# Performance work log

Hardware: AMD Instinct MI355X
Metric: run time of the kernel (lower is better)

The kernel has to match this reference:

```python
import jax, jax.numpy as jnp
import numpy as np

N = 50000
E = 800000
IN_C = 512
HID_C = 128
OUT_C = 16


def setup_inputs() -> dict:
    key = jax.random.key(0)
    k1, k2, k3, k4, k5 = jax.random.split(key, 5)
    x = jax.random.normal(k1, (N, IN_C), dtype=jnp.float32)
    edge_index = jax.random.randint(k2, (2, E), 0, N, dtype=jnp.int64)
    # GCNConv.lin: Linear(in, hid, bias=False); conv bias zero-init but give random for grad coverage
    W1 = jax.random.normal(k3, (HID_C, IN_C), dtype=jnp.float32) / np.sqrt(IN_C)
    b1 = jnp.zeros((HID_C,), dtype=jnp.float32)
    # GCNNet.fc: Linear(hid, out)
    W2 = jax.random.normal(k4, (OUT_C, HID_C), dtype=jnp.float32) / np.sqrt(HID_C)
    b2 = jax.random.normal(k5, (OUT_C,), dtype=jnp.float32) * 0.01
    return {"x": x, "edge_index": edge_index, "W1": W1, "b1": b1, "W2": W2, "b2": b2}


def reference(x, edge_index, W1, b1, W2, b2):
    # Dropout(p=0.5) is identity in eval mode.
    row, col = edge_index[0], edge_index[1]
    h = x @ W1.T                                    # [N, HID_C]
    deg = jax.ops.segment_sum(jnp.ones((E,), dtype=h.dtype), col, num_segments=N)
    # NOTE: source uses deg.pow(0.5) (sqrt, not inv-sqrt) — faithful to the code.
    d = jnp.sqrt(deg)
    norm = d[row] * d[col]                          # [E]
    msg = norm[:, None] * h[row]                    # gather + scale, [E, HID_C]
    agg = jax.ops.segment_sum(msg, col, num_segments=N)  # scatter-add, [N, HID_C]
    conv_out = agg + b1                             # [N, HID_C]
    return conv_out @ W2.T + b2                     # [N, OUT_C]
```

## Files before the change

kernel.cpp:

```cpp
#include <hip/hip_runtime.h>
#include <hip/hip_bf16.h>
#include <hip/hip_fp16.h>

#define IN_C 512
#define HID_C 128
#define OUT_C 16
#define STILE 8192
#define SSH  13
#define KCH_H 16

typedef float    f32x4 __attribute__((ext_vector_type(4)));
typedef float    f32x2 __attribute__((ext_vector_type(2)));
typedef int      i32x4 __attribute__((ext_vector_type(4)));
typedef _Float16 h16x2 __attribute__((ext_vector_type(2)));

__device__ inline void pk_atomic_add_f16(h16x2* addr, h16x2 val) {
#if __has_builtin(__builtin_amdgcn_global_atomic_fadd_v2f16)
    __builtin_amdgcn_global_atomic_fadd_v2f16(addr, val);
#else
    unsigned int* ap = (unsigned int*)addr;
    unsigned int old = *ap, assumed;
    do {
        assumed = old;
        h16x2 cur = __builtin_bit_cast(h16x2, assumed);
        h16x2 nv = cur + val;
        old = atomicCAS(ap, assumed, __builtin_bit_cast(unsigned int, nv));
    } while (old != assumed);
#endif
}

__global__ __launch_bounds__(256) void prep_hist_kernel(
        const float* __restrict__ W1, const float* __restrict__ b1,
        const float* __restrict__ W2, const float* __restrict__ b2,
        float* __restrict__ Wc, float* __restrict__ cconst,
        const int* __restrict__ ei, int* __restrict__ phist, int E) {
    __shared__ int h[STILE];
    if (blockIdx.x < 32) {
        int idx = blockIdx.x * 256 + threadIdx.x;
        int o = idx >> 9;
        int k = idx & 511;
        float s = 0.f;
#pragma unroll 8
        for (int hh = 0; hh < HID_C; ++hh)
            s = fmaf(W2[o * HID_C + hh], W1[hh * IN_C + k], s);
        Wc[o * IN_C + k] = s;
        return;
    }
    if (blockIdx.x == 32) {
        if (threadIdx.x < OUT_C) {
            int o = threadIdx.x;
            float s = b2[o];
            for (int hh = 0; hh < HID_C; ++hh)
                s = fmaf(b1[hh], W2[o * HID_C + hh], s);
            cconst[o] = s;
        }
        return;
    }
    const int hb = blockIdx.x - 33;
    const int st = hb / KCH_H;
    const int k = hb - st * KCH_H;
    for (int i = threadIdx.x; i < STILE; i += 256) h[i] = 0;
    __syncthreads();

    const int chunk = (((E + KCH_H - 1) / KCH_H) + 3) & ~3;
    const int beg = k * chunk;
    const int end = min(E, beg + chunk);
    const int* cols = ei + E;

    const int nv = (end > beg) ? ((end - beg) >> 2) : 0;
    const i32x4* cv = (const i32x4*)(cols + beg);
    for (int i = threadIdx.x; i < nv; i += 256) {
        i32x4 c = cv[i];
#pragma unroll
        for (int j = 0; j < 4; ++j) {
            int cj = c[j];
            if ((cj >> SSH) == st) atomicAdd(&h[cj & (STILE - 1)], 1);
        }
    }
    for (int e = beg + (nv << 2) + threadIdx.x; e < end; e += 256) {
        int cj = cols[e];
        if ((cj >> SSH) == st) atomicAdd(&h[cj & (STILE - 1)], 1);
    }
    __syncthreads();
    int* outp = phist + (size_t)hb * STILE;
    for (int i = threadIdx.x; i < STILE; i += 256) outp[i] = h[i];
}

__global__ void dsq_zero_kernel(const int* __restrict__ phist, float* __restrict__ dsq,
                                unsigned int* __restrict__ agg32, int N, int aggWords) {
    int i = blockIdx.x * 256 + threadIdx.x;
    if (i < N) {
        int st = i >> SSH, ii = i & (STILE - 1);
        const int* p = phist + (size_t)st * KCH_H * STILE + ii;
        int s = 0;
#pragma unroll
        for (int k = 0; k < KCH_H; ++k) s += p[k * STILE];
        dsq[i] = sqrtf((float)s);
    }
    if (i < aggWords) agg32[i] = 0u;
}

__global__ __launch_bounds__(256) void h2_kernel(const float* __restrict__ x,
                                                 const float* __restrict__ WcG,
                                                 const float* __restrict__ dsq,
                                                 _Float16* __restrict__ h2h, int N) {
    __shared__ float wl[16 * IN_C];
    for (int i = threadIdx.x; i < (16 * IN_C) / 4; i += 256)
        ((f32x4*)wl)[i] = ((const f32x4*)WcG)[i];
    __syncthreads();

    const int lane = threadIdx.x & 63;
    const int wid = (blockIdx.x * 256 + threadIdx.x) >> 6;
    const int nw  = (gridDim.x * 256) >> 6;

    for (int r0 = wid * 4; r0 < N; r0 += nw * 4) {
        const int rmax = min(4, N - r0);
        f32x4 a0[4], a1[4];
#pragma unroll
        for (int rr = 0; rr < 4; ++rr) {
            int r = r0 + (rr < rmax ? rr : 0);
            a0[rr] = *(const f32x4*)(x + (size_t)r * IN_C + 4 * lane);
            a1[rr] = *(const f32x4*)(x + (size_t)r * IN_C + 256 + 4 * lane);
        }
        float p[4][16];
#pragma unroll
        for (int oo = 0; oo < 16; ++oo) {
            f32x4 w0 = *(const f32x4*)(wl + oo * IN_C + 4 * lane);
            f32x4 w1 = *(const f32x4*)(wl + oo * IN_C + 256 + 4 * lane);
#pragma unroll
            for (int rr = 0; rr < 4; ++rr) {
                float s = a0[rr].x * w0.x;
                s = fmaf(a0[rr].y, w0.y, s);
                s = fmaf(a0[rr].z, w0.z, s);
                s = fmaf(a0[rr].w, w0.w, s);
                s = fmaf(a1[rr].x, w1.x, s);
                s = fmaf(a1[rr].y, w1.y, s);
                s = fmaf(a1[rr].z, w1.z, s);
                s = fmaf(a1[rr].w, w1.w, s);
                p[rr][oo] = s;
            }
        }
        float v[4];
#pragma unroll
        for (int rr = 0; rr < 4; ++rr) {
#define RSTEP(MASK, HALF)                                              \
            {                                                          \
                const bool hi = (lane & MASK) != 0;                    \
                _Pragma("unroll")                                      \
                for (int ii = 0; ii < HALF; ++ii) {                    \
                    float send = hi ? p[rr][ii] : p[rr][ii + HALF];    \
                    float recv = __shfl_xor(send, MASK, 64);           \
                    float keep = hi ? p[rr][ii + HALF] : p[rr][ii];    \
                    p[rr][ii] = keep + recv;                           \
                }                                                      \
            }
            RSTEP(1, 8)
            RSTEP(2, 4)
            RSTEP(4, 2)
            RSTEP(8, 1)
#undef RSTEP
            v[rr] = p[rr][0];
        }
        const bool h16 = (lane & 16) != 0;
        float sA = h16 ? v[0] : v[1];
        float mA = (h16 ? v[1] : v[0]) + __shfl_xor(sA, 16, 64);
        float sB = h16 ? v[2] : v[3];
        float mB = (h16 ? v[3] : v[2]) + __shfl_xor(sB, 16, 64);
        const bool h32 = (lane & 32) != 0;
        float sC = h32 ? mA : mB;
        float f  = (h32 ? mB : mA) + __shfl_xor(sC, 32, 64);
        const int qq = lane >> 4, jj = lane & 15;
        const int oo = ((jj & 1) << 3) | ((jj & 2) << 1) | ((jj & 4) >> 1) | ((jj & 8) >> 3);
        if (qq < rmax) {
            int r = r0 + qq;
            h2h[(size_t)r * OUT_C + oo] = (_Float16)(f * dsq[r]);
        }
    }
}

__global__ __launch_bounds__(256) void edge_kernel(const int* __restrict__ ei,
                                                   const _Float16* __restrict__ h2h,
                                                   h16x2* __restrict__ agg, int E) {
    int t = blockIdx.x * 256 + threadIdx.x;
    int e = t >> 3;
    if (e >= E) return;
    int op = t & 7;
    int r = ei[e];
    int c = ei[E + e];
    h16x2 h = *(const h16x2*)(h2h + (size_t)r * OUT_C + (op << 1));
    pk_atomic_add_f16(&agg[(size_t)c * 8 + op], h);
}

__global__ void final_kernel(const h16x2* __restrict__ agg, const float* __restrict__ dsq,
                             const float* __restrict__ cconst, float* __restrict__ out,
                             int words) {
    int i = blockIdx.x * 256 + threadIdx.x;
    if (i >= words) return;
    int n = i >> 3;
    int o = (i & 7) << 1;
    h16x2 a = agg[i];
    float d = dsq[n];
    f32x2 r;
    r.x = fmaf(d, (float)a.x, cconst[o]);
    r.y = fmaf(d, (float)a.y, cconst[o + 1]);
    *(f32x2*)(out + ((size_t)i << 1)) = r;
}

extern "C" void kernel_launch(void* const* d_in, const int* in_sizes, int n_in,
                              void* d_out, int out_size, void* d_ws, size_t ws_size,
                              hipStream_t stream) {
    const float* x  = (const float*)d_in[0];
    const int*   ei = (const int*)d_in[1];
    const float* W1 = (const float*)d_in[2];
    const float* b1 = (const float*)d_in[3];
    const float* W2 = (const float*)d_in[4];
    const float* b2 = (const float*)d_in[5];
    float* out = (float*)d_out;

    const int N = in_sizes[0] / IN_C;
    const int E = in_sizes[1] / 2;
    const int ST = (N + STILE - 1) / STILE;
    const int aggWords = (N * OUT_C) / 2;

    float* ws     = (float*)d_ws;
    float* Wc     = ws;
    float* cconst = ws + 16 * IN_C;
    float* dsq    = cconst + 16;
    _Float16* h2h = (_Float16*)(dsq + N);
    int*   phist  = (int*)((unsigned int*)(dsq + N) + 8 * (size_t)N);
    unsigned int* agg32 = (unsigned int*)(phist + (size_t)ST * KCH_H * STILE);
    h16x2* agg = (h16x2*)agg32;

    hipLaunchKernelGGL(prep_hist_kernel, dim3(33 + ST * KCH_H), dim3(256), 0, stream,
                       W1, b1, W2, b2, Wc, cconst, ei, phist, E);
    hipLaunchKernelGGL(dsq_zero_kernel, dim3((aggWords + 255) / 256), dim3(256), 0, stream,
                       phist, dsq, agg32, N, aggWords);
    hipLaunchKernelGGL(h2_kernel, dim3(768), dim3(256), 0, stream, x, Wc, dsq, h2h, N);
    hipLaunchKernelGGL(edge_kernel, dim3((E * 8 + 255) / 256), dim3(256), 0, stream,
                       ei, h2h, agg, E);
    hipLaunchKernelGGL(final_kernel, dim3((aggWords + 255) / 256), dim3(256), 0, stream,
                       agg, dsq, cconst, out, aggWords);
}
```

Before: 101.9 us.

## Fold degree reduction into h2 kernel and agg zeroing into prep launch

Removes the separate dsq_zero kernel. Zeroing of the aggregation buffer moves into extra blocks of the prep/histogram launch. The per-node degree sum and sqrt are now computed inside h2_kernel with a wave shuffle reduction over the partial histograms. The histogram split doubles to 32 chunks and the h2 grid grows, which trades one kernel launch and a dependency for more partial-histogram traffic and extra work inside the GEMV kernel.

```diff
diff --git a/kernel.cpp b/kernel.cpp
--- a/kernel.cpp
+++ b/kernel.cpp
@@ -7,7 +7,7 @@
 #define OUT_C 16
 #define STILE 8192
 #define SSH  13
-#define KCH_H 16
+#define KCH_H 32
 
 typedef float    f32x4 __attribute__((ext_vector_type(4)));
 typedef float    f32x2 __attribute__((ext_vector_type(2)));
@@ -33,7 +33,8 @@
         const float* __restrict__ W1, const float* __restrict__ b1,
         const float* __restrict__ W2, const float* __restrict__ b2,
         float* __restrict__ Wc, float* __restrict__ cconst,
-        const int* __restrict__ ei, int* __restrict__ phist, int E) {
+        const int* __restrict__ ei, int* __restrict__ phist,
+        unsigned int* __restrict__ agg32, int E, int nhist, int aggWords) {
     __shared__ int h[STILE];
     if (blockIdx.x < 32) {
         int idx = blockIdx.x * 256 + threadIdx.x;
@@ -56,6 +57,11 @@
         }
         return;
     }
+    if (blockIdx.x >= 33 + nhist) {
+        int i = (blockIdx.x - 33 - nhist) * 256 + threadIdx.x;
+        if (i < aggWords) agg32[i] = 0u;
+        return;
+    }
     const int hb = blockIdx.x - 33;
     const int st = hb / KCH_H;
     const int k = hb - st * KCH_H;
@@ -86,23 +92,10 @@
     for (int i = threadIdx.x; i < STILE; i += 256) outp[i] = h[i];
 }
 
-__global__ void dsq_zero_kernel(const int* __restrict__ phist, float* __restrict__ dsq,
-                                unsigned int* __restrict__ agg32, int N, int aggWords) {
-    int i = blockIdx.x * 256 + threadIdx.x;
-    if (i < N) {
-        int st = i >> SSH, ii = i & (STILE - 1);
-        const int* p = phist + (size_t)st * KCH_H * STILE + ii;
-        int s = 0;
-#pragma unroll
-        for (int k = 0; k < KCH_H; ++k) s += p[k * STILE];
-        dsq[i] = sqrtf((float)s);
-    }
-    if (i < aggWords) agg32[i] = 0u;
-}
-
 __global__ __launch_bounds__(256) void h2_kernel(const float* __restrict__ x,
                                                  const float* __restrict__ WcG,
-                                                 const float* __restrict__ dsq,
+                                                 const int* __restrict__ phist,
+                                                 float* __restrict__ dsq,
                                                  _Float16* __restrict__ h2h, int N) {
     __shared__ float wl[16 * IN_C];
     for (int i = threadIdx.x; i < (16 * IN_C) / 4; i += 256)
@@ -115,6 +108,20 @@
 
     for (int r0 = wid * 4; r0 < N; r0 += nw * 4) {
         const int rmax = min(4, N - r0);
+
+        const int rr_d = lane >> 4;
+        const int rd = min(r0 + rr_d, N - 1);
+        const int std = rd >> SSH, id = rd & (STILE - 1);
+        const int kd = lane & 15;
+        const int* pb = phist + ((size_t)std * KCH_H) * STILE + id;
+        int deg = pb[(size_t)kd * STILE] + pb[(size_t)(kd + 16) * STILE];
+        deg += __shfl_xor(deg, 1, 64);
+        deg += __shfl_xor(deg, 2, 64);
+        deg += __shfl_xor(deg, 4, 64);
+        deg += __shfl_xor(deg, 8, 64);
+        const float dsq_r = sqrtf((float)deg);
+        if (kd == 0 && rr_d < rmax) dsq[r0 + rr_d] = dsq_r;
+
         f32x4 a0[4], a1[4];
 #pragma unroll
         for (int rr = 0; rr < 4; ++rr) {
@@ -173,7 +180,7 @@
         const int oo = ((jj & 1) << 3) | ((jj & 2) << 1) | ((jj & 4) >> 1) | ((jj & 8) >> 3);
         if (qq < rmax) {
             int r = r0 + qq;
-            h2h[(size_t)r * OUT_C + oo] = (_Float16)(f * dsq[r]);
+            h2h[(size_t)r * OUT_C + oo] = (_Float16)(f * dsq_r);
         }
     }
 }
@@ -220,6 +227,7 @@
     const int N = in_sizes[0] / IN_C;
     const int E = in_sizes[1] / 2;
     const int ST = (N + STILE - 1) / STILE;
+    const int nhist = ST * KCH_H;
     const int aggWords = (N * OUT_C) / 2;
 
     float* ws     = (float*)d_ws;
@@ -231,11 +239,10 @@
     unsigned int* agg32 = (unsigned int*)(phist + (size_t)ST * KCH_H * STILE);
     h16x2* agg = (h16x2*)agg32;
 
-    hipLaunchKernelGGL(prep_hist_kernel, dim3(33 + ST * KCH_H), dim3(256), 0, stream,
-                       W1, b1, W2, b2, Wc, cconst, ei, phist, E);
-    hipLaunchKernelGGL(dsq_zero_kernel, dim3((aggWords + 255) / 256), dim3(256), 0, stream,
-                       phist, dsq, agg32, N, aggWords);
-    hipLaunchKernelGGL(h2_kernel, dim3(768), dim3(256), 0, stream, x, Wc, dsq, h2h, N);
+    const int zblocks = (aggWords + 255) / 256;
+    hipLaunchKernelGGL(prep_hist_kernel, dim3(33 + nhist + zblocks), dim3(256), 0, stream,
+                       W1, b1, W2, b2, Wc, cconst, ei, phist, agg32, E, nhist, aggWords);
+    hipLaunchKernelGGL(h2_kernel, dim3(1024), dim3(256), 0, stream, x, Wc, phist, dsq, h2h, N);
     hipLaunchKernelGGL(edge_kernel, dim3((E * 8 + 255) / 256), dim3(256), 0, stream,
                        ei, h2h, agg, E);
     hipLaunchKernelGGL(final_kernel, dim3((aggWords + 255) / 256), dim3(256), 0, stream,
```

After: 90.84 us. 1.12x faster.
